# Performance work log

Measured on AMD Instinct MI355X. Metric: run time of the kernel, lower is better.

Reference implementation:

```python
import jax, jax.numpy as jnp
import numpy as np

H, DH, M = 8, 64, 3          # heads, dim_head, num memory tokens
DIM = 512                    # model dim
INNER = H * DH               # 512
SCALE = DH ** -0.5
SQRT_DH = float(np.sqrt(DH))
SQRT_M = float(np.sqrt(M))


def setup_inputs() -> dict:
    key = jax.random.key(0)
    ks = jax.random.split(key, 7)
    b, n = 2, 2048
    x = jax.random.normal(ks[0], (b, n, DIM), dtype=jnp.float32)
    # Linear weights stored as (in, out); y = x @ W
    wq = jax.random.normal(ks[1], (DIM, INNER), dtype=jnp.float32) * (DIM ** -0.5)
    wkv = jax.random.normal(ks[2], (DIM, 2 * INNER), dtype=jnp.float32) * (DIM ** -0.5)
    wo = jax.random.normal(ks[3], (INNER, DIM), dtype=jnp.float32) * (INNER ** -0.5)
    bo = jnp.zeros((DIM,), dtype=jnp.float32)
    # xavier_normal_ std = sqrt(2 / (fan_in + fan_out)) over last two dims (M, INNER)
    xav = float(np.sqrt(2.0 / (M + INNER)))
    m_k = jax.random.normal(ks[4], (1, M, INNER), dtype=jnp.float32) * xav
    m_v = jax.random.normal(ks[5], (1, M, INNER), dtype=jnp.float32) * xav
    return {"x": x, "wq": wq, "wkv": wkv, "wo": wo, "bo": bo, "m_k": m_k, "m_v": m_v}


def reference(x, wq, wkv, wo, bo, m_k, m_v):
    b, n, _ = x.shape
    # projections -> (b, h, n, d)
    q = (x @ wq).reshape(b, n, H, DH).transpose(0, 2, 1, 3)
    kv = x @ wkv
    k, v = jnp.split(kv, 2, axis=-1)
    k = k.reshape(b, n, H, DH).transpose(0, 2, 1, 3)
    v = v.reshape(b, n, H, DH).transpose(0, 2, 1, 3)
    # memory tokens: torch does expand(b, M, INNER).view(b, H, M, DH),
    # a flat reshape (NOT a per-head rearrange) -- replicate exactly.
    mk = SQRT_DH * jnp.broadcast_to(m_k, (b, M, INNER)).reshape(b, H, M, DH)
    mv = SQRT_M * jnp.broadcast_to(m_v, (b, M, INNER)).reshape(b, H, M, DH)
    k = jnp.concatenate([k, mk], axis=2)  # (b, h, n+M, d)
    v = jnp.concatenate([v, mv], axis=2)
    dots = jnp.einsum('bhid,bhjd->bhij', q, k) * SCALE  # (b, h, n, n+M)
    attn = jax.nn.softmax(dots, axis=-1)                # dropout = identity (eval)
    out = jnp.einsum('bhij,bhjd->bhid', attn, v)
    out = out.transpose(0, 2, 1, 3).reshape(b, n, INNER)
    return out @ wo + bo
```

## Files before the change

### kernel.cpp

```cpp
#include <hip/hip_runtime.h>

typedef unsigned short u16;
typedef unsigned int u32;
typedef __attribute__((ext_vector_type(8))) __bf16 bf16x8;
typedef __attribute__((ext_vector_type(4))) float f32x4;

#define DEVI __device__ __forceinline__
#define SMAX 16.0f

DEVI float bf2f(u16 u) {
    unsigned int v = ((unsigned int)u) << 16;
    return __uint_as_float(v);
}
DEVI u16 f2bf(float f) {
    unsigned int x = __float_as_uint(f);
    x += 0x7fffu + ((x >> 16) & 1u);
    return (u16)(x >> 16);
}
DEVI u32 pk2(float lo, float hi) {
    union { __bf16 b[2]; u32 u; } c;
    c.b[0] = (__bf16)lo; c.b[1] = (__bf16)hi;
    return c.u;
}
DEVI bf16x8 ldb8(const u16* p) {
    union { uint4 u; bf16x8 b; } c;
    c.u = *(const uint4*)p;
    return c.b;
}
DEVI f32x4 mfma32(bf16x8 a, bf16x8 b, f32x4 c) {
    return __builtin_amdgcn_mfma_f32_16x16x32_bf16(a, b, c, 0, 0, 0);
}
DEVI float clamp4(float v) { return fminf(fmaxf(v, -1e4f), 1e4f); }

__global__ __launch_bounds__(256) void prep(
    const float* __restrict__ wq, const float* __restrict__ wkv,
    const float* __restrict__ wo, const float* __restrict__ x,
    const float* __restrict__ mkf, const float* __restrict__ mvf,
    u16* __restrict__ wqkvT, u16* __restrict__ woT, u16* __restrict__ xb,
    u16* __restrict__ qkv)
{
    const int bid = blockIdx.x, tid = threadIdx.x;
    if (bid < 256) {
        __shared__ u16 T[64][68];
        int j0, k0; const float* W; int ldw; u16* Out;
        if (bid < 192) { int jt = bid % 24, kt = bid / 24;
            j0 = jt * 64; k0 = kt * 64;
            if (j0 < 512) { W = wq + j0;          ldw = 512;  }
            else          { W = wkv + (j0 - 512); ldw = 1024; }
            Out = wqkvT;
        } else { int t = bid - 192;
            j0 = (t >> 3) * 64; k0 = (t & 7) * 64;
            W = wo + j0; ldw = 512; Out = woT;
        }
        const int lr = tid >> 4, lc = tid & 15;
        #pragma unroll
        for (int i = 0; i < 4; ++i) {
            int k = lr + i * 16;
            float4 v = *(const float4*)(W + (size_t)(k0 + k) * ldw + lc * 4);
            u16 p[4] = { f2bf(v.x), f2bf(v.y), f2bf(v.z), f2bf(v.w) };
            *(uint2*)&T[k][lc * 4] = *(uint2*)p;
        }
        __syncthreads();
        #pragma unroll
        for (int i = 0; i < 4; ++i) {
            int j = lr + i * 16;
            u16 p[4];
            #pragma unroll
            for (int c = 0; c < 4; ++c) p[c] = T[lc * 4 + c][j];
            *(uint2*)(Out + (size_t)(j0 + j) * 512 + k0 + lc * 4) = *(uint2*)p;
        }
    } else if (bid < 2304) {
        int e = (bid - 256) * 1024 + tid * 4;
        float4 v = *(const float4*)(x + e);
        u16 p[4] = { f2bf(v.x), f2bf(v.y), f2bf(v.z), f2bf(v.w) };
        *(uint2*)(xb + e) = *(uint2*)p;
    } else {
        int e = (bid - 2304) * 256 + tid;
        int b = e >> 16, rem = e & 65535;
        int row2 = rem >> 10, c = rem & 1023;
        float v = 0.f;
        if (row2 < 3) {
            int hh = (c & 511) >> 6, d = c & 63;
            int src = hh * 192 + row2 * 64 + d;
            v = (c < 512) ? 8.0f * mkf[src] : 1.7320508f * mvf[src];
        }
        qkv[((size_t)b * 2112 + 2048 + row2) * 1536 + 512 + c] = f2bf(v);
    }
}

template<bool F32OUT>
__global__ __launch_bounds__(256) void gemm_bt(
    const u16* __restrict__ A, int lda,
    const u16* __restrict__ BT, int ldb,
    void* __restrict__ Cv, int ldc,
    const float* __restrict__ bias, int K, int mpad)
{
    __shared__ alignas(16) u16 As[64][72];
    __shared__ alignas(16) u16 Bs[64][72];

    const int tid = threadIdx.x;
    const int m0 = blockIdx.x * 64, n0 = blockIdx.y * 64;
    const int w = tid >> 6, lane = tid & 63, l15 = lane & 15, quad = lane >> 4;
    const int srow = tid >> 2, scg = (tid & 3) * 16;

    f32x4 acc[4];
    for (int t = 0; t < 4; ++t) acc[t] = (f32x4){0.f, 0.f, 0.f, 0.f};

    const u16* ap = A + (size_t)(m0 + srow) * lda + scg;
    const u16* bp = BT + (size_t)(n0 + srow) * ldb + scg;

    for (int k0 = 0; k0 < K; k0 += 64) {
        uint4 a0 = *(const uint4*)ap, a1 = *(const uint4*)(ap + 8);
        uint4 b0 = *(const uint4*)bp, b1 = *(const uint4*)(bp + 8);
        ap += 64; bp += 64;
        __syncthreads();
        *(uint4*)&As[srow][scg]     = a0;
        *(uint4*)&As[srow][scg + 8] = a1;
        *(uint4*)&Bs[srow][scg]     = b0;
        *(uint4*)&Bs[srow][scg + 8] = b1;
        __syncthreads();
        #pragma unroll
        for (int ks = 0; ks < 2; ++ks) {
            bf16x8 af = ldb8(&As[16 * w + l15][ks * 32 + quad * 8]);
            #pragma unroll
            for (int t = 0; t < 4; ++t) {
                bf16x8 bf = ldb8(&Bs[16 * t + l15][ks * 32 + quad * 8]);
                acc[t] = mfma32(af, bf, acc[t]);
            }
        }
    }

    #pragma unroll
    for (int t = 0; t < 4; ++t) {
        int col = n0 + 16 * t + l15;
        float bv = bias ? bias[col] : 0.f;
        #pragma unroll
        for (int r = 0; r < 4; ++r) {
            int row = m0 + 16 * w + quad * 4 + r;
            int orow = row + ((row >> 11) * mpad);
            float vr = clamp4(acc[t][r] + bv);
            if (F32OUT) ((float*)Cv)[(size_t)orow * ldc + col] = vr;
            else        ((u16*)Cv)[(size_t)orow * ldc + col] = f2bf(vr);
        }
    }
}

__global__ __launch_bounds__(256, 5) void attn_kernel(
    const u16* __restrict__ qkv, u16* __restrict__ Opart,
    float* __restrict__ Lpart)
{
    __shared__ alignas(16) u16 Ks[64][72];
    __shared__ alignas(16) u16 Vt[64][72];
    __shared__ alignas(16) u16 Ps[64][72];

    const int tid = threadIdx.x;
    const int bx = blockIdx.x;
    const int qt = bx / 5, s = bx - qt * 5;
    const int h = blockIdx.y, b = blockIdx.z;
    const int w = tid >> 6, lane = tid & 63, l15 = lane & 15, quad = lane >> 4;
    const size_t bq = (size_t)b * 2112;
    const int rq = qt * 64;
    const int ro = b * 2048 + qt * 64;

    {
        int row = tid >> 2, cg = (tid & 3) * 16;
        const u16* src = qkv + (bq + rq + row) * 1536 + h * 64 + cg;
        *(uint4*)&Ks[row][cg]     = *(const uint4*)src;
        *(uint4*)&Ks[row][cg + 8] = *(const uint4*)(src + 8);
    }
    __syncthreads();
    bf16x8 qf[2];
    qf[0] = ldb8(&Ks[16 * w + l15][quad * 8]);
    qf[1] = ldb8(&Ks[16 * w + l15][32 + quad * 8]);

    f32x4 O[4];
    for (int t = 0; t < 4; ++t) O[t] = (f32x4){0.f, 0.f, 0.f, 0.f};
    float l_lane = 0.f;

    const int krow = tid >> 2, kcg = (tid & 3) * 16;
    const int vkp = (tid & 31) * 2, vdg = ((tid >> 5) & 7) * 8;

    const int kt0 = 7 * s - (s > 3 ? s - 3 : 0);
    const int kt1 = kt0 + (s < 3 ? 7 : 6);
    for (int kt = kt0; kt < kt1; ++kt) {
        __syncthreads();
        const u16* ksrc = qkv + (bq + kt * 64 + krow) * 1536 + 512 + h * 64 + kcg;
        uint4 k0 = *(const uint4*)ksrc, k1 = *(const uint4*)(ksrc + 8);
        const u16* vsrc = qkv + (bq + kt * 64 + vkp) * 1536 + 1024 + h * 64 + vdg;
        uint4 v0 = *(const uint4*)vsrc, v1 = *(const uint4*)(vsrc + 1536);
        *(uint4*)&Ks[krow][kcg]     = k0;
        *(uint4*)&Ks[krow][kcg + 8] = k1;
        {
            u32 a0[4] = {v0.x, v0.y, v0.z, v0.w};
            u32 a1[4] = {v1.x, v1.y, v1.z, v1.w};
            #pragma unroll
            for (int i = 0; i < 4; ++i) {
                u32 lo = __builtin_amdgcn_perm(a1[i], a0[i], 0x05040100u);
                u32 hi = __builtin_amdgcn_perm(a1[i], a0[i], 0x07060302u);
                *(u32*)&Vt[vdg + 2 * i][vkp]     = lo;
                *(u32*)&Vt[vdg + 2 * i + 1][vkp] = hi;
            }
        }
        __syncthreads();

        f32x4 d4[4];
        for (int t = 0; t < 4; ++t) d4[t] = (f32x4){0.f, 0.f, 0.f, 0.f};
        #pragma unroll
        for (int ks = 0; ks < 2; ++ks) {
            #pragma unroll
            for (int t = 0; t < 4; ++t) {
                bf16x8 kf = ldb8(&Ks[16 * t + l15][ks * 32 + quad * 8]);
                d4[t] = mfma32(kf, qf[ks], d4[t]);
            }
        }
        if (kt == 32) {
            #pragma unroll
            for (int t = 1; t < 4; ++t)
                d4[t] = (f32x4){-1e9f, -1e9f, -1e9f, -1e9f};
            #pragma unroll
            for (int r = 0; r < 4; ++r)
                if (!(quad == 0 && r < 3)) d4[0][r] = -1e9f;
        }

        #pragma unroll
        for (int t = 0; t < 4; ++t) {
            float p0 = __expf(fmaf(d4[t][0], 0.125f, -SMAX));
            float p1 = __expf(fmaf(d4[t][1], 0.125f, -SMAX));
            float p2 = __expf(fmaf(d4[t][2], 0.125f, -SMAX));
            float p3 = __expf(fmaf(d4[t][3], 0.125f, -SMAX));
            l_lane += (p0 + p1) + (p2 + p3);
            uint2 pv = { pk2(p0, p1), pk2(p2, p3) };
            *(uint2*)&Ps[16 * w + l15][16 * t + 4 * quad] = pv;
        }
        #pragma unroll
        for (int ks = 0; ks < 2; ++ks) {
            bf16x8 af = ldb8(&Ps[16 * w + l15][ks * 32 + quad * 8]);
            #pragma unroll
            for (int dt = 0; dt < 4; ++dt) {
                bf16x8 vf = ldb8(&Vt[16 * dt + l15][ks * 32 + quad * 8]);
                O[dt] = mfma32(af, vf, O[dt]);
            }
        }
    }

    l_lane += __shfl_xor(l_lane, 16, 64);
    l_lane += __shfl_xor(l_lane, 32, 64);
    u16* Ob = Opart + (size_t)s * 4096 * 512;
    #pragma unroll
    for (int r = 0; r < 4; ++r) {
        int row = ro + 16 * w + quad * 4 + r;
        #pragma unroll
        for (int dt = 0; dt < 4; ++dt)
            Ob[(size_t)row * 512 + h * 64 + 16 * dt + l15] = f2bf(O[dt][r]);
    }
    if (lane < 16)
        Lpart[((size_t)s * 4096 + ro + 16 * w + lane) * 8 + h] = l_lane;
}

__global__ __launch_bounds__(256) void merge_kernel(
    const u16* __restrict__ Opart, const float* __restrict__ Lpart,
    u16* __restrict__ outp)
{
    int e = (blockIdx.x * 256 + threadIdx.x) * 4;
    int row = e >> 9, h = (e & 511) >> 6;
    float ax = 0.f, ay = 0.f, az = 0.f, aw = 0.f, l = 0.f;
    #pragma unroll
    for (int s = 0; s < 5; ++s) {
        uint2 pv = *(const uint2*)(Opart + (size_t)s * 4096 * 512 + e);
        ax += bf2f((u16)(pv.x & 0xffff)); ay += bf2f((u16)(pv.x >> 16));
        az += bf2f((u16)(pv.y & 0xffff)); aw += bf2f((u16)(pv.y >> 16));
        l += Lpart[((size_t)s * 4096 + row) * 8 + h];
    }
    float rl = 1.0f / fmaxf(l, 1e-30f);
    u16 p[4] = { f2bf(clamp4(ax * rl)), f2bf(clamp4(ay * rl)),
                 f2bf(clamp4(az * rl)), f2bf(clamp4(aw * rl)) };
    *(uint2*)(outp + e) = *(uint2*)p;
}

extern "C" void kernel_launch(void* const* d_in, const int* in_sizes, int n_in,
                              void* d_out, int out_size, void* d_ws, size_t ws_size,
                              hipStream_t stream)
{
    (void)in_sizes; (void)n_in; (void)out_size; (void)ws_size;
    const float* x   = (const float*)d_in[0];
    const float* wq  = (const float*)d_in[1];
    const float* wkv = (const float*)d_in[2];
    const float* wo  = (const float*)d_in[3];
    const float* bo  = (const float*)d_in[4];
    const float* mk  = (const float*)d_in[5];
    const float* mv  = (const float*)d_in[6];
    float* out = (float*)d_out;

    u16* qkv   = (u16*)d_ws;
    u16* outp  = qkv + 6488064;
    u16* woT   = outp + 2097152;
    float* Lpart = (float*)(woT + 262144);
    u16* scratch = (u16*)(Lpart + 163840);
    u16* wqkvT = scratch;
    u16* xb    = scratch + 786432;
    u16* Opart = scratch;

    prep<<<2816, 256, 0, stream>>>(wq, wkv, wo, x, mk, mv, wqkvT, woT, xb, qkv);
    gemm_bt<false><<<dim3(64, 24), 256, 0, stream>>>(xb, 512, wqkvT, 512,
                                                     qkv, 1536, nullptr, 512, 64);
    attn_kernel<<<dim3(160, 8, 2), 256, 0, stream>>>(qkv, Opart, Lpart);
    merge_kernel<<<2048, 256, 0, stream>>>(Opart, Lpart, outp);
    gemm_bt<true><<<dim3(64, 8), 256, 0, stream>>>(outp, 512, woT, 512,
                                                   out, 512, bo, 512, 0);
}
```

Baseline: 142.2 us.

## Use 128-row GEMM tiles with direct-to-LDS loads; fold softmax denominator into MFMA

Replaces both projection GEMMs with a 128xTN tiled kernel that loads operands straight into LDS via global_load_lds and gives each wave a 4xWNT MFMA block, raising reuse per LDS fetch. In attention, the row-sum of probabilities is now computed by an extra MFMA against a ones row in Vt instead of per-lane adds and shuffles, and exp is rewritten as a native exp2 with prescaled constants. The K-step drops to 32 with two barriers per step, which may expose load latency, and the ones-row sum uses bf16-rounded probabilities.

```diff
diff --git a/kernel.cpp b/kernel.cpp
--- a/kernel.cpp
+++ b/kernel.cpp
@@ -6,7 +6,8 @@
 typedef __attribute__((ext_vector_type(4))) float f32x4;
 
 #define DEVI __device__ __forceinline__
-#define SMAX 16.0f
+#define C1 0.180336880f
+#define C2 (-23.0831200f)
 
 DEVI float bf2f(u16 u) {
     unsigned int v = ((unsigned int)u) << 16;
@@ -31,6 +32,12 @@
     return __builtin_amdgcn_mfma_f32_16x16x32_bf16(a, b, c, 0, 0, 0);
 }
 DEVI float clamp4(float v) { return fminf(fmaxf(v, -1e4f), 1e4f); }
+DEVI float fexp2(float x) { return __builtin_amdgcn_exp2f(x); }
+DEVI void gld16(const u16* g, u16* l) {
+    __builtin_amdgcn_global_load_lds(
+        (const __attribute__((address_space(1))) void*)g,
+        (__attribute__((address_space(3))) void*)l, 16, 0, 0);
+}
 
 __global__ __launch_bounds__(256) void prep(
     const float* __restrict__ wq, const float* __restrict__ wkv,
@@ -88,59 +95,72 @@
     }
 }
 
-template<bool F32OUT>
-__global__ __launch_bounds__(256) void gemm_bt(
+template<int WNT, bool F32OUT>
+__global__ __launch_bounds__(256) void gemm128(
     const u16* __restrict__ A, int lda,
     const u16* __restrict__ BT, int ldb,
     void* __restrict__ Cv, int ldc,
     const float* __restrict__ bias, int K, int mpad)
 {
-    __shared__ alignas(16) u16 As[64][72];
-    __shared__ alignas(16) u16 Bs[64][72];
+    constexpr int TN = 32 * WNT;
+    __shared__ u16 As[128 * 32];
+    __shared__ u16 Bs[TN * 32];
 
     const int tid = threadIdx.x;
-    const int m0 = blockIdx.x * 64, n0 = blockIdx.y * 64;
+    const int m0 = blockIdx.x * 128, n0 = blockIdx.y * TN;
     const int w = tid >> 6, lane = tid & 63, l15 = lane & 15, quad = lane >> 4;
-    const int srow = tid >> 2, scg = (tid & 3) * 16;
-
-    f32x4 acc[4];
-    for (int t = 0; t < 4; ++t) acc[t] = (f32x4){0.f, 0.f, 0.f, 0.f};
-
-    const u16* ap = A + (size_t)(m0 + srow) * lda + scg;
-    const u16* bp = BT + (size_t)(n0 + srow) * ldb + scg;
-
-    for (int k0 = 0; k0 < K; k0 += 64) {
-        uint4 a0 = *(const uint4*)ap, a1 = *(const uint4*)(ap + 8);
-        uint4 b0 = *(const uint4*)bp, b1 = *(const uint4*)(bp + 8);
-        ap += 64; bp += 64;
-        __syncthreads();
-        *(uint4*)&As[srow][scg]     = a0;
-        *(uint4*)&As[srow][scg + 8] = a1;
-        *(uint4*)&Bs[srow][scg]     = b0;
-        *(uint4*)&Bs[srow][scg + 8] = b1;
-        __syncthreads();
-        #pragma unroll
-        for (int ks = 0; ks < 2; ++ks) {
-            bf16x8 af = ldb8(&As[16 * w + l15][ks * 32 + quad * 8]);
-            #pragma unroll
-            for (int t = 0; t < 4; ++t) {
-                bf16x8 bf = ldb8(&Bs[16 * t + l15][ks * 32 + quad * 8]);
-                acc[t] = mfma32(af, bf, acc[t]);
+    const int wr = w >> 1, wc = w & 1;
+
+    const int srow = w * 16 + (lane >> 2), scg = (lane & 3) * 8;
+
+    f32x4 acc[4][WNT];
+    #pragma unroll
+    for (int i = 0; i < 4; ++i)
+        #pragma unroll
+        for (int j = 0; j < WNT; ++j) acc[i][j] = (f32x4){0.f, 0.f, 0.f, 0.f};
+
+    const u16* aG0 = A + (size_t)(m0 + srow) * lda + scg;
+    const u16* aG1 = A + (size_t)(m0 + 64 + srow) * lda + scg;
+    const u16* bG0 = BT + (size_t)(n0 + srow) * ldb + scg;
+    const u16* bG1 = (WNT == 4) ? BT + (size_t)(n0 + 64 + srow) * ldb + scg : bG0;
+
+    for (int k0 = 0; k0 < K; k0 += 32) {
+        __syncthreads();
+        gld16(aG0, &As[w * 512]);
+        gld16(aG1, &As[2048 + w * 512]);
+        gld16(bG0, &Bs[w * 512]);
+        if (WNT == 4) gld16(bG1, &Bs[2048 + w * 512]);
+        aG0 += 32; aG1 += 32; bG0 += 32; bG1 += 32;
+        __syncthreads();
+
+        bf16x8 af[4], bf[WNT];
+        #pragma unroll
+        for (int i = 0; i < 4; ++i)
+            af[i] = ldb8(&As[(wr * 64 + 16 * i + l15) * 32 + quad * 8]);
+        #pragma unroll
+        for (int j = 0; j < WNT; ++j)
+            bf[j] = ldb8(&Bs[(wc * (TN / 2) + 16 * j + l15) * 32 + quad * 8]);
+        #pragma unroll
+        for (int i = 0; i < 4; ++i)
+            #pragma unroll
+            for (int j = 0; j < WNT; ++j)
+                acc[i][j] = mfma32(af[i], bf[j], acc[i][j]);
+    }
+
+    #pragma unroll
+    for (int j = 0; j < WNT; ++j) {
+        int col = n0 + wc * (TN / 2) + 16 * j + l15;
+        float bv = bias ? bias[col] : 0.f;
+        #pragma unroll
+        for (int i = 0; i < 4; ++i) {
+            #pragma unroll
+            for (int r = 0; r < 4; ++r) {
+                int row = m0 + wr * 64 + 16 * i + quad * 4 + r;
+                int orow = row + ((row >> 11) * mpad);
+                float vr = clamp4(acc[i][j][r] + bv);
+                if (F32OUT) ((float*)Cv)[(size_t)orow * ldc + col] = vr;
+                else        ((u16*)Cv)[(size_t)orow * ldc + col] = f2bf(vr);
             }
-        }
-    }
-
-    #pragma unroll
-    for (int t = 0; t < 4; ++t) {
-        int col = n0 + 16 * t + l15;
-        float bv = bias ? bias[col] : 0.f;
-        #pragma unroll
-        for (int r = 0; r < 4; ++r) {
-            int row = m0 + 16 * w + quad * 4 + r;
-            int orow = row + ((row >> 11) * mpad);
-            float vr = clamp4(acc[t][r] + bv);
-            if (F32OUT) ((float*)Cv)[(size_t)orow * ldc + col] = vr;
-            else        ((u16*)Cv)[(size_t)orow * ldc + col] = f2bf(vr);
         }
     }
 }
@@ -150,7 +170,7 @@
     float* __restrict__ Lpart)
 {
     __shared__ alignas(16) u16 Ks[64][72];
-    __shared__ alignas(16) u16 Vt[64][72];
+    __shared__ alignas(16) u16 Vt[80][72];
     __shared__ alignas(16) u16 Ps[64][72];
 
     const int tid = threadIdx.x;
@@ -163,6 +183,11 @@
     const int ro = b * 2048 + qt * 64;
 
     {
+        int row = 64 + (tid >> 4), col = (tid & 15) * 4;
+        uint2 ones = { 0x3F803F80u, 0x3F803F80u };
+        *(uint2*)&Vt[row][col] = ones;
+    }
+    {
         int row = tid >> 2, cg = (tid & 3) * 16;
         const u16* src = qkv + (bq + rq + row) * 1536 + h * 64 + cg;
         *(uint4*)&Ks[row][cg]     = *(const uint4*)src;
@@ -173,9 +198,9 @@
     qf[0] = ldb8(&Ks[16 * w + l15][quad * 8]);
     qf[1] = ldb8(&Ks[16 * w + l15][32 + quad * 8]);
 
-    f32x4 O[4];
+    f32x4 O[4], O5;
     for (int t = 0; t < 4; ++t) O[t] = (f32x4){0.f, 0.f, 0.f, 0.f};
-    float l_lane = 0.f;
+    O5 = (f32x4){0.f, 0.f, 0.f, 0.f};
 
     const int krow = tid >> 2, kcg = (tid & 3) * 16;
     const int vkp = (tid & 31) * 2, vdg = ((tid >> 5) & 7) * 8;
@@ -224,11 +249,10 @@
 
         #pragma unroll
         for (int t = 0; t < 4; ++t) {
-            float p0 = __expf(fmaf(d4[t][0], 0.125f, -SMAX));
-            float p1 = __expf(fmaf(d4[t][1], 0.125f, -SMAX));
-            float p2 = __expf(fmaf(d4[t][2], 0.125f, -SMAX));
-            float p3 = __expf(fmaf(d4[t][3], 0.125f, -SMAX));
-            l_lane += (p0 + p1) + (p2 + p3);
+            float p0 = fexp2(fmaf(d4[t][0], C1, C2));
+            float p1 = fexp2(fmaf(d4[t][1], C1, C2));
+            float p2 = fexp2(fmaf(d4[t][2], C1, C2));
+            float p3 = fexp2(fmaf(d4[t][3], C1, C2));
             uint2 pv = { pk2(p0, p1), pk2(p2, p3) };
             *(uint2*)&Ps[16 * w + l15][16 * t + 4 * quad] = pv;
         }
@@ -240,11 +264,11 @@
                 bf16x8 vf = ldb8(&Vt[16 * dt + l15][ks * 32 + quad * 8]);
                 O[dt] = mfma32(af, vf, O[dt]);
             }
-        }
-    }
-
-    l_lane += __shfl_xor(l_lane, 16, 64);
-    l_lane += __shfl_xor(l_lane, 32, 64);
+            bf16x8 of = ldb8(&Vt[64 + l15][ks * 32 + quad * 8]);
+            O5 = mfma32(af, of, O5);
+        }
+    }
+
     u16* Ob = Opart + (size_t)s * 4096 * 512;
     #pragma unroll
     for (int r = 0; r < 4; ++r) {
@@ -252,9 +276,9 @@
         #pragma unroll
         for (int dt = 0; dt < 4; ++dt)
             Ob[(size_t)row * 512 + h * 64 + 16 * dt + l15] = f2bf(O[dt][r]);
-    }
-    if (lane < 16)
-        Lpart[((size_t)s * 4096 + ro + 16 * w + lane) * 8 + h] = l_lane;
+        if (l15 == 0)
+            Lpart[((size_t)s * 4096 + row) * 8 + h] = O5[r];
+    }
 }
 
 __global__ __launch_bounds__(256) void merge_kernel(
@@ -301,10 +325,10 @@
     u16* Opart = scratch;
 
     prep<<<2816, 256, 0, stream>>>(wq, wkv, wo, x, mk, mv, wqkvT, woT, xb, qkv);
-    gemm_bt<false><<<dim3(64, 24), 256, 0, stream>>>(xb, 512, wqkvT, 512,
-                                                     qkv, 1536, nullptr, 512, 64);
+    gemm128<4, false><<<dim3(32, 12), 256, 0, stream>>>(
+        xb, 512, wqkvT, 512, qkv, 1536, nullptr, 512, 64);
     attn_kernel<<<dim3(160, 8, 2), 256, 0, stream>>>(qkv, Opart, Lpart);
     merge_kernel<<<2048, 256, 0, stream>>>(Opart, Lpart, outp);
-    gemm_bt<true><<<dim3(64, 8), 256, 0, stream>>>(outp, 512, woT, 512,
-                                                   out, 512, bo, 512, 0);
-}
+    gemm128<2, true><<<dim3(32, 8), 256, 0, stream>>>(
+        outp, 512, woT, 512, out, 512, bo, 512, 0);
+}
```

Result: slower. 145.1 us (+2.0%).
